# Kernel tuning notes

Hardware: AMD Instinct MI355X
Metric: run time of the kernel (lower is better)

The kernel has to match this reference:

```python
import jax, jax.numpy as jnp
import numpy as np

B, T, D_MODEL = 4, 4096, 512
HEADS, BUCKET_SIZE, N_HASHES = 8, 64, 4
DIM_HEAD = D_MODEL // HEADS  # 64
D_FFN = 2048
N_BUCKETS = T // BUCKET_SIZE  # 64
SELF_ATTN_VALUE = -5e4  # reformer TOKEN_SELF_ATTN_VALUE


def setup_inputs() -> dict:
    key = jax.random.key(0)
    ks = jax.random.split(key, 16)
    s = 0.02
    return {
        'x': jax.random.normal(ks[0], (B, T, D_MODEL), jnp.float32),
        'rotations': jax.random.normal(ks[1], (DIM_HEAD, N_HASHES, N_BUCKETS // 2), jnp.float32),
        'w_qk': jax.random.normal(ks[2], (D_MODEL, D_MODEL), jnp.float32) * s,
        'w_v': jax.random.normal(ks[3], (D_MODEL, D_MODEL), jnp.float32) * s,
        'w_out': jax.random.normal(ks[4], (D_MODEL, D_MODEL), jnp.float32) * s,
        'b_out': jnp.zeros((D_MODEL,), jnp.float32),
        'ln1_g': jnp.ones((D_MODEL,), jnp.float32),
        'ln1_b': jnp.zeros((D_MODEL,), jnp.float32),
        'w1': jax.random.normal(ks[5], (D_FFN, D_MODEL), jnp.float32) * s,
        'b1': jnp.zeros((D_FFN,), jnp.float32),
        'w2': jax.random.normal(ks[6], (D_MODEL, D_FFN), jnp.float32) * s,
        'b2': jnp.zeros((D_MODEL,), jnp.float32),
        'ln2_g': jnp.ones((D_MODEL,), jnp.float32),
        'ln2_b': jnp.zeros((D_MODEL,), jnp.float32),
    }


def layer_norm(x, g, b, eps=1e-6):
    m = x.mean(-1, keepdims=True)
    v = ((x - m) ** 2).mean(-1, keepdims=True)
    return (x - m) / jnp.sqrt(v + eps) * g + b


def look_one_back(x):
    # concat each chunk with the previous chunk (wrap-around), along in-chunk axis
    prev = jnp.roll(x, 1, axis=1)
    return jnp.concatenate([x, prev], axis=2)


def lsh_attention(qk, v, rotations):
    # qk, v: (bh, t, d) with shared-QK; rotations: (d, n_hashes, n_buckets//2)
    bh, t, d = qk.shape
    # --- hash: random rotations, argmax over [R, -R] ---
    rot = jnp.einsum('btf,fhi->bhti', qk, rotations)
    rot = jnp.concatenate([rot, -rot], axis=-1)        # (bh, H, t, n_buckets)
    buckets = jnp.argmax(rot, axis=-1)                 # (bh, H, t)
    buckets = buckets + (jnp.arange(N_HASHES) * N_BUCKETS)[None, :, None]
    buckets = buckets.reshape(bh, N_HASHES * t)
    # --- sort by (bucket, position) ---
    ticker = jnp.arange(N_HASHES * t)
    buckets_and_t = t * buckets + (ticker % t)[None, :]
    sticker = jnp.argsort(buckets_and_t, axis=-1)      # stable sort
    undo_sort = jnp.argsort(sticker, axis=-1)
    st = sticker % t                                   # original positions, sorted order
    sqk = jnp.take_along_axis(qk, st[..., None], axis=1)
    sv = jnp.take_along_axis(v, st[..., None], axis=1)
    # --- chunk: n_hashes*n_buckets chunks of bucket_size tokens ---
    n_chunks = N_HASHES * N_BUCKETS
    bq_t = st.reshape(bh, n_chunks, -1)
    bqk = sqk.reshape(bh, n_chunks, -1, d)
    bv = sv.reshape(bh, n_chunks, -1, d)
    bk = bqk / jnp.clip(jnp.linalg.norm(bqk, axis=-1, keepdims=True), 1e-6, None)
    bk = look_one_back(bk)
    bv = look_one_back(bv)
    bkv_t = look_one_back(bq_t)
    # --- local attention within chunk (+ previous chunk) ---
    dots = jnp.einsum('bcid,bcjd->bcij', bqk, bk) * (DIM_HEAD ** -0.5)
    self_mask = bq_t[..., None] == bkv_t[..., None, :]
    dots = jnp.where(self_mask, SELF_ATTN_VALUE, dots)
    logits = jax.nn.logsumexp(dots, axis=-1, keepdims=True)
    probs = jnp.exp(dots - logits)
    bo = jnp.einsum('bcij,bcjd->bcid', probs, bv)
    # --- unsort and combine hash rounds by softmax over round logits ---
    so = bo.reshape(bh, N_HASHES * t, d)
    slogits = logits.reshape(bh, N_HASHES * t)
    o = jnp.take_along_axis(so, undo_sort[..., None], axis=1).reshape(bh, N_HASHES, t, d)
    lg = jnp.take_along_axis(slogits, undo_sort, axis=1).reshape(bh, N_HASHES, t, 1)
    w = jnp.exp(lg - jax.nn.logsumexp(lg, axis=1, keepdims=True))
    return (o * w).sum(axis=1)                         # (bh, t, d)


def reference(x, rotations, w_qk, w_v, w_out, b_out, ln1_g, ln1_b, w1, b1, w2, b2, ln2_g, ln2_b):
    b, t, _ = x.shape
    qk = x @ w_qk.T
    v = x @ w_v.T

    def split_heads(u):
        return u.reshape(b, t, HEADS, DIM_HEAD).transpose(0, 2, 1, 3).reshape(b * HEADS, t, DIM_HEAD)

    attn = lsh_attention(split_heads(qk), split_heads(v), rotations)
    attn = attn.reshape(b, HEADS, t, DIM_HEAD).transpose(0, 2, 1, 3).reshape(b, t, D_MODEL)
    attn = attn @ w_out.T + b_out
    # residual + LN (dropout is identity at inference)
    h = layer_norm(attn + x, ln1_g, ln1_b)
    # position-wise FFN with its own residual + LN
    f = jax.nn.relu(h @ w1.T + b1) @ w2.T + b2
    return layer_norm(f + h, ln2_g, ln2_b)
```

## Files before the change

kernel.cpp:

```cpp
#include <hip/hip_runtime.h>
#include <stdint.h>

typedef unsigned short u16;
typedef __attribute__((ext_vector_type(4))) int   i32x4;
typedef __attribute__((ext_vector_type(4))) float f32x4;

__device__ __forceinline__ u16 f2bf(float x){
  unsigned int u = __float_as_uint(x);
  u += 0x7FFFu + ((u >> 16) & 1u);
  return (u16)(u >> 16);
}
__device__ __forceinline__ float bf2f(u16 h){
  return __uint_as_float(((unsigned int)h) << 16);
}
__device__ __forceinline__ unsigned int cvtpk_bf16(float lo, float hi){
  unsigned int r;
  asm("v_cvt_pk_bf16_f32 %0, %1, %2" : "=v"(r) : "v"(lo), "v"(hi));
  return r;
}
__device__ __forceinline__ f32x4 mfma16(i32x4 a, i32x4 b, f32x4 c){
  asm("v_mfma_f32_16x16x32_bf16 %0, %1, %2, %0" : "+v"(c) : "v"(a), "v"(b));
  return c;
}
__device__ __forceinline__ f32x4 acc_fence(f32x4 c){
  asm volatile("s_nop 7\ns_nop 7" : "+v"(c));
  return c;
}
__device__ __forceinline__ void gl_lds16(const void* g, void* l){
  unsigned long long ga = (unsigned long long)g;
  unsigned int la = (unsigned int)(unsigned long long)l;
  __builtin_amdgcn_global_load_lds((const __attribute__((address_space(1))) void*)ga,
                                   (__attribute__((address_space(3))) void*)la, 16, 0, 0);
}
__device__ __forceinline__ int xcd_swz(int f, int n){
  int chunk = n >> 3;
  return (f & 7) * chunk + (f >> 3);
}
__device__ __forceinline__ unsigned int f2mono(float v){
  unsigned int u = __float_as_uint(v);
  return u ^ ((unsigned int)((int)u >> 31) | 0x80000000u);
}
__device__ __forceinline__ float mono2f(unsigned int mu){
  unsigned int u = (mu & 0x80000000u) ? (mu ^ 0x80000000u) : ~mu;
  return __uint_as_float(u);
}
__device__ __forceinline__ unsigned long long shfl_xor_u64(unsigned long long x, int m){
  int lo = __shfl_xor((int)(unsigned int)(x & 0xFFFFFFFFull), m);
  int hi = __shfl_xor((int)(unsigned int)(x >> 32), m);
  return ((unsigned long long)(unsigned int)hi << 32) | (unsigned int)lo;
}

__global__ __launch_bounds__(256) void k_wprep(
    const float* __restrict__ x,
    const float* __restrict__ w_qk, const float* __restrict__ w_v,
    const float* __restrict__ w_out, const float* __restrict__ w1,
    const float* __restrict__ w2, const float* __restrict__ rot,
    u16* __restrict__ xh, u16* __restrict__ xl,
    u16* __restrict__ wqkh, u16* __restrict__ wqkl,
    u16* __restrict__ wvb, u16* __restrict__ wob,
    u16* __restrict__ w1b, u16* __restrict__ w2b,
    u16* __restrict__ rothi, u16* __restrict__ rotlo)
{
  const int bid = blockIdx.x;
  if (bid < 8192){
    int i = bid*256 + threadIdx.x;
    float4 v = ((const float4*)x)[i];
    ushort4 h, l;
    h.x=f2bf(v.x); l.x=f2bf(v.x - bf2f(h.x));
    h.y=f2bf(v.y); l.y=f2bf(v.y - bf2f(h.y));
    h.z=f2bf(v.z); l.z=f2bf(v.z - bf2f(h.z));
    h.w=f2bf(v.w); l.w=f2bf(v.w - bf2f(h.w));
    ((ushort4*)xh)[i]=h; ((ushort4*)xl)[i]=l;
    return;
  }
  if (bid >= 11008){
    int i = (bid - 11008)*256 + threadIdx.x;
    int d = i & 63, n = i >> 6;
    float v = rot[d*128 + n];
    u16 h = f2bf(v);
    rothi[i] = h; rotlo[i] = f2bf(v - bf2f(h));
    return;
  }
  const int i = (bid - 8192)*256 + threadIdx.x;
  if (i < 65536){
    float4 v = ((const float4*)w_qk)[i];
    ushort4 h, l;
    h.x=f2bf(v.x); l.x=f2bf(v.x - bf2f(h.x));
    h.y=f2bf(v.y); l.y=f2bf(v.y - bf2f(h.y));
    h.z=f2bf(v.z); l.z=f2bf(v.z - bf2f(h.z));
    h.w=f2bf(v.w); l.w=f2bf(v.w - bf2f(h.w));
    ((ushort4*)wqkh)[i]=h; ((ushort4*)wqkl)[i]=l;
    return;
  }
  const float* src; u16* dst; int j;
  if (i < 131072){ src = w_v;  dst = wvb; j = i - 65536; }
  else if (i < 196608){ src = w_out; dst = wob; j = i - 131072; }
  else if (i < 458752){ src = w1;   dst = w1b; j = i - 196608; }
  else { src = w2; dst = w2b; j = i - 458752; }
  float4 v = ((const float4*)src)[j];
  ushort4 o; o.x=f2bf(v.x); o.y=f2bf(v.y); o.z=f2bf(v.z); o.w=f2bf(v.w);
  ((ushort4*)dst)[j] = o;
}

__global__ __launch_bounds__(256) void k_gemm(
    const u16* __restrict__ A0, const u16* __restrict__ B0,
    const float* __restrict__ bias, u16* __restrict__ Cb,
    int M, int N, int K)
{
  const int tid = threadIdx.x;
  const int l = tid & 63, w = tid >> 6;
  const int lr = l & 15, lg = l >> 4;
  int flat = blockIdx.y * gridDim.x + blockIdx.x;
  flat = xcd_swz(flat, gridDim.x * gridDim.y);
  const int m0 = (flat / gridDim.x) * 128, n0 = (flat % gridDim.x) * 128;
  const int mbase = (w >> 1) * 64, nbase = (w & 1) * 64;

  __shared__ __align__(16) u16 As[128*64];
  __shared__ __align__(16) u16 Bs[128*64];

  f32x4 zero = {0.f,0.f,0.f,0.f};
  f32x4 acc[4][4];
  #pragma unroll
  for (int i=0;i<4;i++)
    #pragma unroll
    for (int j=0;j<4;j++) acc[i][j] = zero;

  const int row_s = tid >> 3;
  const int c16   = tid & 7;

  for (int k0 = 0; k0 < K; k0 += 64){
    #pragma unroll
    for (int q=0;q<4;q++){
      int ra = q*32 + row_s;
      int cs = c16 ^ (ra & 7);
      gl_lds16(A0 + (size_t)(m0 + ra)*K + k0 + cs*8, (char*)As + q*4096 + tid*16);
      gl_lds16(B0 + (size_t)(n0 + ra)*K + k0 + cs*8, (char*)Bs + q*4096 + tid*16);
    }
    __syncthreads();
    #pragma unroll
    for (int kk=0; kk<64; kk+=32){
      i32x4 af[4], bfr[4];
      #pragma unroll
      for (int mf=0;mf<4;mf++){
        int row = mbase + mf*16 + lr;
        af[mf] = *(const i32x4*)((const char*)As + row*128 + (((kk*2) + (lg*16)) ^ ((row&7)<<4)));
      }
      #pragma unroll
      for (int nf=0;nf<4;nf++){
        int row = nbase + nf*16 + lr;
        bfr[nf] = *(const i32x4*)((const char*)Bs + row*128 + (((kk*2) + (lg*16)) ^ ((row&7)<<4)));
      }
      #pragma unroll
      for (int mf=0;mf<4;mf++)
        #pragma unroll
        for (int nf=0;nf<4;nf++)
          acc[mf][nf] = mfma16(af[mf], bfr[nf], acc[mf][nf]);
    }
    __syncthreads();
  }

  #pragma unroll
  for (int mf=0;mf<4;mf++){
    #pragma unroll
    for (int nf=0;nf<4;nf++){
      f32x4 v = acc_fence(acc[mf][nf]);
      #pragma unroll
      for (int r=0;r<4;r++){
        int m = m0 + mbase + mf*16 + lg*4 + r;
        int n = n0 + nbase + nf*16 + lr;
        float val = fmaxf(v[r] + bias[n], 0.f);
        Cb[(size_t)m*N + n] = f2bf(val);
      }
    }
  }
}

template<int MODE>
__global__ __launch_bounds__(256, 4) void k_gemm64(
    const u16* __restrict__ A0, const u16* __restrict__ B0,
    const float* __restrict__ bias, u16* __restrict__ Cb,
    int M, int N, int K)
{
  const int tid = threadIdx.x;
  const int l = tid & 63, w = tid >> 6;
  const int lr = l & 15, lg = l >> 4;
  int flat = xcd_swz(blockIdx.x, gridDim.x);
  const int nT = N >> 7;
  const int m0 = (flat / nT) * 64, n0 = (flat % nT) * 128;

  __shared__ __align__(16) u16 As[64*64];
  __shared__ __align__(16) u16 Bs[128*64];

  f32x4 zero = {0.f,0.f,0.f,0.f};
  f32x4 acc[4][2];
  #pragma unroll
  for (int i=0;i<4;i++)
    #pragma unroll
    for (int j=0;j<2;j++) acc[i][j] = zero;

  const int row_s = tid >> 3;
  const int c8    = tid & 7;

  for (int k0 = 0; k0 < K; k0 += 64){
    #pragma unroll
    for (int q=0;q<2;q++){
      int ra = q*32 + row_s;
      int cs = c8 ^ (ra & 7);
      gl_lds16(A0 + (size_t)(m0 + ra)*K + k0 + cs*8, (char*)As + q*4096 + tid*16);
    }
    #pragma unroll
    for (int q=0;q<4;q++){
      int rb = q*32 + row_s;
      int cs = c8 ^ (rb & 7);
      gl_lds16(B0 + (size_t)(n0 + rb)*K + k0 + cs*8, (char*)Bs + q*4096 + tid*16);
    }
    __syncthreads();
    #pragma unroll
    for (int kk=0; kk<64; kk+=32){
      i32x4 af[4], bfr[2];
      #pragma unroll
      for (int mf=0;mf<4;mf++){
        int row = mf*16 + lr;
        af[mf] = *(const i32x4*)((const char*)As + row*128 + (((kk*2) + (lg*16)) ^ ((row&7)<<4)));
      }
      #pragma unroll
      for (int nf=0;nf<2;nf++){
        int row = w*32 + nf*16 + lr;
        bfr[nf] = *(const i32x4*)((const char*)Bs + row*128 + (((kk*2) + (lg*16)) ^ ((row&7)<<4)));
      }
      #pragma unroll
      for (int mf=0;mf<4;mf++)
        #pragma unroll
        for (int nf=0;nf<2;nf++)
          acc[mf][nf] = mfma16(af[mf], bfr[nf], acc[mf][nf]);
    }
    __syncthreads();
  }

  #pragma unroll
  for (int mf=0;mf<4;mf++){
    #pragma unroll
    for (int nf=0;nf<2;nf++){
      f32x4 v = acc_fence(acc[mf][nf]);
      #pragma unroll
      for (int r=0;r<4;r++){
        int m = m0 + mf*16 + lg*4 + r;
        int n = n0 + w*32 + nf*16 + lr;
        float val = v[r];
        if (MODE == 4){
          val += bias[n];
          Cb[(size_t)m*N + n] = f2bf(val);
        } else {
          int b = m >> 12, t = m & 4095, h = n >> 6, d = n & 63;
          size_t pos = (((size_t)(b*8 + h)) << 12) + t;
          Cb[pos*192 + 64 + d] = f2bf(val);
        }
      }
    }
  }
}

__global__ __launch_bounds__(256, 3) void k_gemmqk(
    const u16* __restrict__ Ah, const u16* __restrict__ Al,
    const u16* __restrict__ Bh, const u16* __restrict__ Bl,
    u16* __restrict__ kv, u16* __restrict__ qlo)
{
  const int K = 512;
  const int tid = threadIdx.x;
  const int l = tid & 63, w = tid >> 6;
  const int lr = l & 15, lg = l >> 4;
  int flat = xcd_swz(blockIdx.x, 1024);
  const int m0 = (flat >> 3) * 128, n0 = (flat & 7) * 64;
  const int mbase = w * 32;

  __shared__ __align__(16) u16 AsH[128*64];
  __shared__ __align__(16) u16 AsL[128*64];
  __shared__ __align__(16) u16 BsH[64*64];
  __shared__ __align__(16) u16 BsL[64*64];

  f32x4 zero = {0.f,0.f,0.f,0.f};
  f32x4 acc[2][4];
  #pragma unroll
  for (int i=0;i<2;i++)
    #pragma unroll
    for (int j=0;j<4;j++) acc[i][j] = zero;

  const int row_s = tid >> 3;
  const int c16   = tid & 7;

  for (int k0 = 0; k0 < K; k0 += 64){
    #pragma unroll
    for (int q=0;q<4;q++){
      int ra = q*32 + row_s;
      int cs = c16 ^ (ra & 7);
      size_t ao = (size_t)(m0 + ra)*K + k0 + cs*8;
      gl_lds16(Ah + ao, (char*)AsH + q*4096 + tid*16);
      gl_lds16(Al + ao, (char*)AsL + q*4096 + tid*16);
    }
    #pragma unroll
    for (int q=0;q<2;q++){
      int rb = q*32 + row_s;
      int cs = c16 ^ (rb & 7);
      size_t bo2 = (size_t)(n0 + rb)*K + k0 + cs*8;
      gl_lds16(Bh + bo2, (char*)BsH + q*4096 + tid*16);
      gl_lds16(Bl + bo2, (char*)BsL + q*4096 + tid*16);
    }
    __syncthreads();
    #pragma unroll
    for (int kk=0; kk<64; kk+=32){
      i32x4 ah[2], al[2], bh2[4], bl2[4];
      #pragma unroll
      for (int mf=0;mf<2;mf++){
        int row = mbase + mf*16 + lr;
        int off = (((kk*2) + (lg*16)) ^ ((row&7)<<4));
        ah[mf] = *(const i32x4*)((const char*)AsH + row*128 + off);
        al[mf] = *(const i32x4*)((const char*)AsL + row*128 + off);
      }
      #pragma unroll
      for (int nf=0;nf<4;nf++){
        int row = nf*16 + lr;
        int off = (((kk*2) + (lg*16)) ^ ((row&7)<<4));
        bh2[nf] = *(const i32x4*)((const char*)BsH + row*128 + off);
        bl2[nf] = *(const i32x4*)((const char*)BsL + row*128 + off);
      }
      #pragma unroll
      for (int mf=0;mf<2;mf++)
        #pragma unroll
        for (int nf=0;nf<4;nf++){
          acc[mf][nf] = mfma16(ah[mf], bh2[nf], acc[mf][nf]);
          acc[mf][nf] = mfma16(al[mf], bh2[nf], acc[mf][nf]);
          acc[mf][nf] = mfma16(ah[mf], bl2[nf], acc[mf][nf]);
        }
    }
    __syncthreads();
  }

  const int hh = n0 >> 6;
  #pragma unroll
  for (int mf=0;mf<2;mf++){
    f32x4 v[4];
    #pragma unroll
    for (int nf=0;nf<4;nf++) v[nf] = acc_fence(acc[mf][nf]);
    #pragma unroll
    for (int r=0;r<4;r++){
      float ss = 0.f;
      #pragma unroll
      for (int nf=0;nf<4;nf++) ss += v[nf][r]*v[nf][r];
      ss += __shfl_xor(ss, 1); ss += __shfl_xor(ss, 2);
      ss += __shfl_xor(ss, 4); ss += __shfl_xor(ss, 8);
      float scale = 0.18033688f / fmaxf(sqrtf(ss), 1e-6f);
      int m = m0 + mbase + mf*16 + lg*4 + r;
      int b = m >> 12, t = m & 4095;
      size_t pos = (((size_t)(b*8 + hh)) << 12) + t;
      #pragma unroll
      for (int nf=0;nf<4;nf++){
        float val = v[nf][r];
        u16 hbf = f2bf(val);
        int d = nf*16 + lr;
        kv [pos*192 + d]       = f2bf(val * scale);
        kv [pos*192 + 128 + d] = hbf;
        qlo[pos*64  + d]       = f2bf(val - bf2f(hbf));
      }
    }
  }
}

__global__ __launch_bounds__(256) void k_hash2(
    const u16* __restrict__ kv, const u16* __restrict__ ql,
    const u16* __restrict__ rh, const u16* __restrict__ rl,
    int* __restrict__ bkt)
{
  const int tid = threadIdx.x;
  const int l = tid & 63, w = tid >> 6, lr = l & 15, lg = l >> 4;
  __shared__ __align__(16) u16 Rh[128*64];
  __shared__ __align__(16) u16 Rl[128*64];
  {
    const int row_s = tid >> 3, c8 = tid & 7;
    #pragma unroll
    for (int q = 0; q < 4; q++){
      int ra = q*32 + row_s;
      int cs = c8 ^ (ra & 7);
      gl_lds16(rh + ra*64 + cs*8, (char*)Rh + q*4096 + tid*16);
      gl_lds16(rl + ra*64 + cs*8, (char*)Rl + q*4096 + tid*16);
    }
  }
  const int blk = xcd_swz(blockIdx.x, gridDim.x);
  const int qrow = blk*64 + w*16 + lr;
  const size_t qoff = (size_t)qrow*192 + 128;
  const size_t loff = (size_t)qrow*64;
  i32x4 qhf[2], qlf[2];
  qhf[0] = *(const i32x4*)(kv + qoff + lg*8);
  qhf[1] = *(const i32x4*)(kv + qoff + 32 + lg*8);
  qlf[0] = *(const i32x4*)(ql + loff + lg*8);
  qlf[1] = *(const i32x4*)(ql + loff + 32 + lg*8);
  __syncthreads();

  f32x4 zero = {0.f,0.f,0.f,0.f};
  f32x4 acc[8];
  #pragma unroll
  for (int i=0;i<8;i++) acc[i] = zero;
  #pragma unroll
  for (int ks = 0; ks < 2; ks++){
    #pragma unroll
    for (int nf = 0; nf < 8; nf++){
      int row = nf*16 + lr;
      int off = (ks*64 + lg*16) ^ ((row & 7) << 4);
      i32x4 rhf = *(const i32x4*)((const char*)Rh + row*128 + off);
      i32x4 rlf = *(const i32x4*)((const char*)Rl + row*128 + off);
      acc[nf] = mfma16(rhf, qhf[ks], acc[nf]);
      acc[nf] = mfma16(rlf, qhf[ks], acc[nf]);
      acc[nf] = mfma16(rhf, qlf[ks], acc[nf]);
    }
  }

  const int bh = qrow >> 12, t = qrow & 4095;
  #pragma unroll
  for (int hh = 0; hh < 4; hh++){
    f32x4 v0 = acc_fence(acc[2*hh]);
    f32x4 v1 = acc_fence(acc[2*hh+1]);
    unsigned long long kmax = 0, kmin = 0;
    #pragma unroll
    for (int r = 0; r < 4; r++){
      int j0 = lg*4 + r, j1 = 16 + lg*4 + r;
      unsigned int mu0 = f2mono(v0[r]), mu1 = f2mono(v1[r]);
      unsigned long long a = ((unsigned long long)mu0 << 32) | (unsigned int)(31 - j0);
      unsigned long long b = ((unsigned long long)mu1 << 32) | (unsigned int)(31 - j1);
      if (a > kmax) kmax = a;
      if (b > kmax) kmax = b;
      unsigned long long c = ((unsigned long long)(~mu0) << 32) | (unsigned int)(31 - j0);
      unsigned long long d = ((unsigned long long)(~mu1) << 32) | (unsigned int)(31 - j1);
      if (c > kmin) kmin = c;
      if (d > kmin) kmin = d;
    }
    #pragma unroll
    for (int msk = 16; msk < 64; msk <<= 1){
      unsigned long long o1 = shfl_xor_u64(kmax, msk); if (o1 > kmax) kmax = o1;
      unsigned long long o2 = shfl_xor_u64(kmin, msk); if (o2 > kmin) kmin = o2;
    }
    if (lg == 0){
      float vmax = mono2f((unsigned int)(kmax >> 32));
      int jmax = 31 - (int)(kmax & 0xFFFFFFFFull);
      float vmin = mono2f(~(unsigned int)(kmin >> 32));
      int jmin = 31 - (int)(kmin & 0xFFFFFFFFull);
      int bucket = (vmax >= -vmin) ? jmax : 32 + jmin;
      bkt[((size_t)(bh*4 + hh) << 12) + t] = bucket;
    }
  }
}

__global__ __launch_bounds__(64) void k_sort(const int* __restrict__ buckets, int* __restrict__ st){
  const int grp = blockIdx.x;
  const int t = threadIdx.x;
  __shared__ int bkL[4096];
  __shared__ int hist[64][65];
  __shared__ int tot[64];
  const size_t gbase = ((size_t)grp) << 12;
  for (int i=0;i<64;i++)
    bkL[i*64 + t] = buckets[gbase + i*64 + t];
  #pragma unroll
  for (int b=0;b<64;b++) hist[t][b] = 0;
  __syncthreads();
  for (int i=0;i<64;i++){
    int b = bkL[t*64 + i];
    hist[t][b]++;
  }
  __syncthreads();
  { int run = 0;
    for (int tt=0; tt<64; tt++){ int v = hist[tt][t]; hist[tt][t] = run; run += v; }
    tot[t] = run; }
  __syncthreads();
  { int v = tot[t]; int incl = v;
    #pragma unroll
    for (int d=1; d<64; d<<=1){ int n = __shfl_up(incl, d, 64); if (t >= d) incl += n; }
    tot[t] = incl - v; }
  __syncthreads();
  const size_t obase = (((size_t)(grp>>2)) << 14) + ((size_t)(grp&3) << 12);
  for (int i=0;i<64;i++){
    int e = t*64 + i;
    int b = bkL[e];
    int dest = tot[b] + hist[t][b];
    hist[t][b]++;
    st[obase + dest] = e;
  }
}

__global__ __launch_bounds__(256, 5) void k_attn(
    const u16* __restrict__ kv,
    const int* __restrict__ st, float* __restrict__ lgt_out, u16* __restrict__ bo)
{
  int flat = blockIdx.y * gridDim.x + blockIdx.x;
  flat = xcd_swz(flat, gridDim.x * gridDim.y);
  const int c = flat & 255, bh = flat >> 8;
  const int rnd = c >> 6;
  const int cprev = (c + 255) & 255;
  const int tid = threadIdx.x;
  const int l = tid & 63, w = tid >> 6, lr = l & 15, lg = l >> 4;

  __shared__ __align__(16) u16 Ks[128*64];
  __shared__ __align__(16) u16 Vt[64*128];

  const size_t stbase = ((size_t)bh) << 14;
  const size_t kvbase = (((size_t)bh) << 12) * 192;

  {
    const int rsub = l >> 3, c8 = l & 7;
    #pragma unroll
    for (int q2 = 0; q2 < 4; q2++){
      int row = w*32 + q2*8 + rsub;
      int cc = (row < 64) ? c : cprev;
      int pos = st[stbase + (cc << 6) + (row & 63)];
      int cs = c8 ^ (row & 7);
      gl_lds16(kv + kvbase + (size_t)pos*192 + cs*8,
               (char*)Ks + (w*4 + q2)*1024 + l*16);
    }
  }

  const int pos_q16 = st[stbase + (c << 6) + (w*16 + lr)];
  i32x4 qf[2];
  #pragma unroll
  for (int ks = 0; ks < 2; ks++)
    qf[ks] = *(const i32x4*)(kv + kvbase + (size_t)pos_q16*192 + 128 + ks*32 + lg*8);

  {
    const int pp = tid & 63, db = tid >> 6;
    const int q5 = pp & 15;
    const int K0 = (pp >> 4)*32 + 16*((q5 >> 1) & 1) + 4*(q5 >> 2) + 2*(q5 & 1);
    int cc0 = (K0 < 64) ? c : cprev;
    int p0 = st[stbase + (cc0 << 6) + (K0 & 63)];
    int p1 = st[stbase + (cc0 << 6) + ((K0 + 1) & 63)];
    const u16* r0 = kv + kvbase + (size_t)p0*192 + 64 + db*16;
    const u16* r1 = kv + kvbase + (size_t)p1*192 + 64 + db*16;
    uint4 a0 = *(const uint4*)r0, a1 = *(const uint4*)(r0 + 8);
    uint4 b0 = *(const uint4*)r1, b1 = *(const uint4*)(r1 + 8);
    uint av[8] = {a0.x,a0.y,a0.z,a0.w,a1.x,a1.y,a1.z,a1.w};
    uint bv[8] = {b0.x,b0.y,b0.z,b0.w,b1.x,b1.y,b1.z,b1.w};
    #pragma unroll
    for (int dd = 0; dd < 16; dd++){
      uint lo = (av[dd>>1] >> ((dd&1)*16)) & 0xFFFFu;
      uint hi = (bv[dd>>1] >> ((dd&1)*16)) & 0xFFFFu;
      int row = db*16 + dd;
      *(uint*)((char*)Vt + row*256 + ((pp*4) ^ ((row & 7) << 5))) = lo | (hi << 16);
    }
  }
  const bool bdry = (c & 63) == 0;
  int pkprev[4][4];
  if (bdry){
    #pragma unroll
    for (int nf2=0; nf2<4; nf2++)
      #pragma unroll
      for (int r=0;r<4;r++)
        pkprev[nf2][r] = st[stbase + (cprev << 6) + nf2*16 + lg*4 + r];
  }
  __syncthreads();

  f32x4 zero = {0.f,0.f,0.f,0.f};
  f32x4 s[8];
  #pragma unroll
  for (int i=0;i<8;i++) s[i] = zero;
  __builtin_amdgcn_s_setprio(1);
  #pragma unroll
  for (int ks = 0; ks < 2; ks++){
    #pragma unroll
    for (int nf = 0; nf < 8; nf++){
      int row = nf*16 + lr;
      i32x4 kf = *(const i32x4*)((const char*)Ks + row*128 + ((ks*64 + lg*16) ^ ((row&7)<<4)));
      s[nf] = mfma16(kf, qf[ks], s[nf]);
    }
  }
  __builtin_amdgcn_s_setprio(0);

  float p[8][4];
  float sum = 0.f;
  #pragma unroll
  for (int nf=0;nf<8;nf++){
    f32x4 t = acc_fence(s[nf]);
    #pragma unroll
    for (int r=0;r<4;r++){
      float e = __builtin_amdgcn_exp2f(t[r]);
      if (nf == w && (lg*4 + r) == lr) e = 0.f;
      if (nf >= 4 && bdry && pkprev[nf-4][r] == pos_q16) e = 0.f;
      p[nf][r] = e;
      sum += e;
    }
  }
  sum += __shfl_xor(sum, 16);
  sum += __shfl_xor(sum, 32);
  float lv = logf(sum);
  float inv = 1.f / sum;
  if (l < 16)
    lgt_out[((((size_t)bh) << 12) + pos_q16)*4 + rnd] = lv;

  i32x4 pa[4];
  #pragma unroll
  for (int ks=0;ks<4;ks++){
    uint w0 = cvtpk_bf16(p[2*ks][0],   p[2*ks][1]);
    uint w1 = cvtpk_bf16(p[2*ks][2],   p[2*ks][3]);
    uint w2 = cvtpk_bf16(p[2*ks+1][0], p[2*ks+1][1]);
    uint w3 = cvtpk_bf16(p[2*ks+1][2], p[2*ks+1][3]);
    i32x4 t = {(int)w0,(int)w1,(int)w2,(int)w3};
    pa[ks] = t;
  }

  f32x4 o[4];
  #pragma unroll
  for (int i=0;i<4;i++) o[i] = zero;
  __builtin_amdgcn_s_setprio(1);
  #pragma unroll
  for (int ks=0;ks<4;ks++){
    #pragma unroll
    for (int nf=0;nf<4;nf++){
      int row = nf*16 + lr;
      i32x4 vf = *(const i32x4*)((const char*)Vt + row*256 + ((ks*64 + lg*16) ^ ((row & 7) << 5)));
      o[nf] = mfma16(pa[ks], vf, o[nf]);
    }
  }
  __builtin_amdgcn_s_setprio(0);
  float invq[4]; int posq[4];
  #pragma unroll
  for (int r=0;r<4;r++){
    invq[r] = __shfl(inv, lg*4 + r, 64);
    posq[r] = __shfl(pos_q16, lg*4 + r, 64);
  }
  #pragma unroll
  for (int nf=0;nf<4;nf++){
    f32x4 ov = acc_fence(o[nf]);
    #pragma unroll
    for (int r=0;r<4;r++){
      bo[((((size_t)bh << 12) + posq[r]))*256 + rnd*64 + nf*16 + lr] = f2bf(ov[r] * invq[r]);
    }
  }
}

__global__ __launch_bounds__(256) void k_combine(const u16* __restrict__ bo, const float* __restrict__ lgt,
                                                 u16* __restrict__ attn){
  const int wid = blockIdx.x * 4 + (threadIdx.x >> 6);
  const int l = threadIdx.x & 63;
  const int bh = wid >> 12, t = wid & 4095;
  const size_t tb = (((size_t)bh) << 12) + t;
  float4 lg4 = *(const float4*)(lgt + tb*4);
  float m = fmaxf(fmaxf(lg4.x,lg4.y), fmaxf(lg4.z,lg4.w));
  float w0 = __expf(lg4.x-m), w1 = __expf(lg4.y-m), w2 = __expf(lg4.z-m), w3 = __expf(lg4.w-m);
  float inv = 1.f / (w0+w1+w2+w3);
  const u16* bp = bo + tb*256;
  float o = w0 * bf2f(bp[l]) + w1 * bf2f(bp[64+l]) + w2 * bf2f(bp[128+l]) + w3 * bf2f(bp[192+l]);
  o *= inv;
  int b = bh >> 3, h = bh & 7;
  attn[((((size_t)b) << 12) + t) * 512 + h*64 + l] = f2bf(o);
}

template<int RESF>
__global__ __launch_bounds__(256) void k_ln(const u16* __restrict__ a,
                                            const float* __restrict__ resf, const u16* __restrict__ resb,
                                            const float* __restrict__ g, const float* __restrict__ bb,
                                            float* __restrict__ of, u16* __restrict__ ob){
  const int row = blockIdx.x*4 + (threadIdx.x >> 6);
  const int l = threadIdx.x & 63;
  const size_t base = (size_t)row*512 + l*8;
  uint4 aa = *(const uint4*)(a + base);
  uint aw[4] = {aa.x, aa.y, aa.z, aa.w};
  float av[8];
  #pragma unroll
  for (int j=0;j<4;j++){
    av[2*j]   = bf2f((u16)(aw[j] & 0xFFFF));
    av[2*j+1] = bf2f((u16)(aw[j] >> 16));
  }
  float rv[8];
  if (RESF){
    float4 r0 = *(const float4*)(resf + base);
    float4 r1 = *(const float4*)(resf + base + 4);
    rv[0]=r0.x; rv[1]=r0.y; rv[2]=r0.z; rv[3]=r0.w;
    rv[4]=r1.x; rv[5]=r1.y; rv[6]=r1.z; rv[7]=r1.w;
  } else {
    uint4 rr = *(const uint4*)(resb + base);
    uint rw[4] = {rr.x, rr.y, rr.z, rr.w};
    #pragma unroll
    for (int j=0;j<4;j++){
      rv[2*j]   = bf2f((u16)(rw[j] & 0xFFFF));
      rv[2*j+1] = bf2f((u16)(rw[j] >> 16));
    }
  }
  float v[8];
  #pragma unroll
  for (int j=0;j<8;j++) v[j] = av[j] + rv[j];
  float sum = 0.f;
  #pragma unroll
  for (int j=0;j<8;j++) sum += v[j];
  #pragma unroll
  for (int msk=1; msk<64; msk<<=1) sum += __shfl_xor(sum, msk);
  float mean = sum * (1.f/512.f);
  float ss = 0.f;
  #pragma unroll
  for (int j=0;j<8;j++){ float d = v[j]-mean; ss += d*d; }
  #pragma unroll
  for (int msk=1; msk<64; msk<<=1) ss += __shfl_xor(ss, msk);
  float rstd = rsqrtf(ss * (1.f/512.f) + 1e-6f);
  float4 g0 = *(const float4*)(g + l*8),  g1 = *(const float4*)(g + l*8 + 4);
  float4 b0 = *(const float4*)(bb + l*8), b1 = *(const float4*)(bb + l*8 + 4);
  float gv[8] = {g0.x,g0.y,g0.z,g0.w,g1.x,g1.y,g1.z,g1.w};
  float bv[8] = {b0.x,b0.y,b0.z,b0.w,b1.x,b1.y,b1.z,b1.w};
  float y[8];
  #pragma unroll
  for (int j=0;j<8;j++) y[j] = (v[j]-mean)*rstd*gv[j] + bv[j];
  if (RESF){
    #pragma unroll
    for (int j=0;j<8;j++) ob[base+j] = f2bf(y[j]);
  } else {
    #pragma unroll
    for (int j=0;j<8;j++) of[base+j] = y[j];
  }
}

extern "C" void kernel_launch(void* const* d_in, const int* in_sizes, int n_in,
                              void* d_out, int out_size, void* d_ws, size_t ws_size,
                              hipStream_t stream) {
  const float* x     = (const float*)d_in[0];
  const float* rot   = (const float*)d_in[1];
  const float* w_qk  = (const float*)d_in[2];
  const float* w_v   = (const float*)d_in[3];
  const float* w_out = (const float*)d_in[4];
  const float* b_out = (const float*)d_in[5];
  const float* ln1_g = (const float*)d_in[6];
  const float* ln1_b = (const float*)d_in[7];
  const float* w1    = (const float*)d_in[8];
  const float* b1    = (const float*)d_in[9];
  const float* w2    = (const float*)d_in[10];
  const float* b2    = (const float*)d_in[11];
  const float* ln2_g = (const float*)d_in[12];
  const float* ln2_b = (const float*)d_in[13];
  float* out = (float*)d_out;

  char* p = (char*)d_ws;
  u16*   xh   = (u16*)(p);
  u16*   xl   = (u16*)(p + 16777216);
  u16*   wqkh = (u16*)(p + 33554432);
  u16*   wqkl = (u16*)(p + 34078720);
  u16*   wvb  = (u16*)(p + 34603008);
  u16*   wob  = (u16*)(p + 35127296);
  u16*   w1b  = (u16*)(p + 35651584);
  u16*   w2b  = (u16*)(p + 37748736);
  u16*   kvb  = (u16*)(p + 39845888);
  int*   bkt  = (int*)(p + 90177536);
  int*   stb  = (int*)(p + 92274688);
  float* lgt  = (float*)(p + 94371840);
  u16*   bo   = (u16*)(p + 96468992);
  u16*   qlo   = bo;
  u16*   rothi = (u16*)(p + 96468992 + 16777216);
  u16*   rotlo = (u16*)(p + 96468992 + 16777216 + 16384);
  u16*   attnc = xl;
  u16*   projb = kvb;
  u16*   fb    = xl;
  u16*   hb    = xh;
  u16*   hid   = bo;

  k_wprep<<<11040, 256, 0, stream>>>(x, w_qk, w_v, w_out, w1, w2, rot,
                                     xh, xl, wqkh, wqkl, wvb, wob, w1b, w2b, rothi, rotlo);
  k_gemmqk<<<1024, 256, 0, stream>>>(xh, xl, wqkh, wqkl, kvb, qlo);
  k_gemm64<3><<<1024, 256, 0, stream>>>(xh, wvb, nullptr, kvb, 16384, 512, 512);
  k_hash2<<<2048, 256, 0, stream>>>(kvb, qlo, rothi, rotlo, bkt);
  k_sort<<<128, 64, 0, stream>>>(bkt, stb);
  k_attn<<<dim3(256,32), 256, 0, stream>>>(kvb, stb, lgt, bo);
  k_combine<<<32768, 256, 0, stream>>>(bo, lgt, attnc);
  k_gemm64<4><<<1024, 256, 0, stream>>>(attnc, wob, b_out, projb, 16384, 512, 512);
  k_ln<1><<<4096, 256, 0, stream>>>(projb, x, nullptr, ln1_g, ln1_b, nullptr, hb);
  k_gemm<<<dim3(16,128), 256, 0, stream>>>(hb, w1b, b1, hid, 16384, 2048, 512);
  k_gemm64<4><<<1024, 256, 0, stream>>>(hid, w2b, b2, fb, 16384, 512, 2048);
  k_ln<0><<<4096, 256, 0, stream>>>(fb, nullptr, hb, ln2_g, ln2_b, out, nullptr);
}
```

Before: 286.7 us.

## Process two adjacent chunks per attention block, reusing shared K/V rows

Each attention workgroup now handles two consecutive sorted chunks instead of one. The current chunk's keys are moved into the 'previous' half of LDS, so only the new chunk's 64 rows are gathered. The next chunk's V and Q are prefetched while the current softmax runs. This halves the gather traffic for the look-one-back keys and overlaps loads with compute, at the cost of more registers (launch bounds lowered to 4 waves) and half as many blocks.

Result: no change. 288.9 us (+0.8%).

```diff
diff --git a/kernel.cpp b/kernel.cpp
--- a/kernel.cpp
+++ b/kernel.cpp
@@ -484,15 +484,12 @@
   }
 }
 
-__global__ __launch_bounds__(256, 5) void k_attn(
+__global__ __launch_bounds__(256, 4) void k_attn(
     const u16* __restrict__ kv,
     const int* __restrict__ st, float* __restrict__ lgt_out, u16* __restrict__ bo)
 {
-  int flat = blockIdx.y * gridDim.x + blockIdx.x;
-  flat = xcd_swz(flat, gridDim.x * gridDim.y);
-  const int c = flat & 255, bh = flat >> 8;
-  const int rnd = c >> 6;
-  const int cprev = (c + 255) & 255;
+  int flat = xcd_swz(blockIdx.x, 4096);
+  const int cpair = flat & 127, bh = flat >> 7;
   const int tid = threadIdx.x;
   const int l = tid & 63, w = tid >> 6, lr = l & 15, lg = l >> 4;
 
@@ -502,8 +499,15 @@
   const size_t stbase = ((size_t)bh) << 14;
   const size_t kvbase = (((size_t)bh) << 12) * 192;
 
+  const int rsub = l >> 3, c8 = l & 7;
+  const int pp = tid & 63, db = tid >> 6;
+  const int q5 = pp & 15;
+  const int K0 = (pp >> 4)*32 + 16*((q5 >> 1) & 1) + 4*(q5 >> 2) + 2*(q5 & 1);
+
+  int c = cpair*2;
+
   {
-    const int rsub = l >> 3, c8 = l & 7;
+    const int cprev = (c + 255) & 255;
     #pragma unroll
     for (int q2 = 0; q2 < 4; q2++){
       int row = w*32 + q2*8 + rsub;
@@ -513,18 +517,6 @@
       gl_lds16(kv + kvbase + (size_t)pos*192 + cs*8,
                (char*)Ks + (w*4 + q2)*1024 + l*16);
     }
-  }
-
-  const int pos_q16 = st[stbase + (c << 6) + (w*16 + lr)];
-  i32x4 qf[2];
-  #pragma unroll
-  for (int ks = 0; ks < 2; ks++)
-    qf[ks] = *(const i32x4*)(kv + kvbase + (size_t)pos_q16*192 + 128 + ks*32 + lg*8);
-
-  {
-    const int pp = tid & 63, db = tid >> 6;
-    const int q5 = pp & 15;
-    const int K0 = (pp >> 4)*32 + 16*((q5 >> 1) & 1) + 4*(q5 >> 2) + 2*(q5 & 1);
     int cc0 = (K0 < 64) ? c : cprev;
     int p0 = st[stbase + (cc0 << 6) + (K0 & 63)];
     int p1 = st[stbase + (cc0 << 6) + ((K0 + 1) & 63)];
@@ -542,9 +534,14 @@
       *(uint*)((char*)Vt + row*256 + ((pp*4) ^ ((row & 7) << 5))) = lo | (hi << 16);
     }
   }
-  const bool bdry = (c & 63) == 0;
+  int pos_q = st[stbase + (c << 6) + (w*16 + lr)];
+  i32x4 qf[2];
+  qf[0] = *(const i32x4*)(kv + kvbase + (size_t)pos_q*192 + 128 + lg*8);
+  qf[1] = *(const i32x4*)(kv + kvbase + (size_t)pos_q*192 + 128 + 32 + lg*8);
+  bool bdry = (c & 63) == 0;
   int pkprev[4][4];
   if (bdry){
+    const int cprev = (c + 255) & 255;
     #pragma unroll
     for (int nf2=0; nf2<4; nf2++)
       #pragma unroll
@@ -553,80 +550,139 @@
   }
   __syncthreads();
 
-  f32x4 zero = {0.f,0.f,0.f,0.f};
-  f32x4 s[8];
-  #pragma unroll
-  for (int i=0;i<8;i++) s[i] = zero;
-  __builtin_amdgcn_s_setprio(1);
-  #pragma unroll
-  for (int ks = 0; ks < 2; ks++){
-    #pragma unroll
-    for (int nf = 0; nf < 8; nf++){
-      int row = nf*16 + lr;
-      i32x4 kf = *(const i32x4*)((const char*)Ks + row*128 + ((ks*64 + lg*16) ^ ((row&7)<<4)));
-      s[nf] = mfma16(kf, qf[ks], s[nf]);
-    }
-  }
-  __builtin_amdgcn_s_setprio(0);
-
-  float p[8][4];
-  float sum = 0.f;
-  #pragma unroll
-  for (int nf=0;nf<8;nf++){
-    f32x4 t = acc_fence(s[nf]);
+  int pos_q_n = 0;
+  i32x4 qfn[2];
+  uint avn[8], bvn[8];
+
+  #pragma unroll
+  for (int it = 0; it < 2; ++it){
+    const int rnd = c >> 6;
+    f32x4 zero = {0.f,0.f,0.f,0.f};
+    f32x4 s[8];
+    #pragma unroll
+    for (int i=0;i<8;i++) s[i] = zero;
+    __builtin_amdgcn_s_setprio(1);
+    #pragma unroll
+    for (int ks = 0; ks < 2; ks++){
+      #pragma unroll
+      for (int nf = 0; nf < 8; nf++){
+        int row = nf*16 + lr;
+        i32x4 kf = *(const i32x4*)((const char*)Ks + row*128 + ((ks*64 + lg*16) ^ ((row&7)<<4)));
+        s[nf] = mfma16(kf, qf[ks], s[nf]);
+      }
+    }
+    __builtin_amdgcn_s_setprio(0);
+
+    if (it == 0){
+      i32x4 kmv0 = *(const i32x4*)((const char*)Ks + tid*32);
+      i32x4 kmv1 = *(const i32x4*)((const char*)Ks + tid*32 + 16);
+      __syncthreads();
+      *(i32x4*)((char*)Ks + 8192 + tid*32)      = kmv0;
+      *(i32x4*)((char*)Ks + 8192 + tid*32 + 16) = kmv1;
+      const int c1 = c + 1;
+      #pragma unroll
+      for (int q2 = 0; q2 < 4; q2++){
+        int row = w*32 + q2*8 + rsub;
+        if (row < 64){
+          int pos = st[stbase + (c1 << 6) + row];
+          int cs = c8 ^ (row & 7);
+          gl_lds16(kv + kvbase + (size_t)pos*192 + cs*8,
+                   (char*)Ks + (w*4 + q2)*1024 + l*16);
+        }
+      }
+      {
+        int cc0 = (K0 < 64) ? c1 : c;
+        int p0 = st[stbase + (cc0 << 6) + (K0 & 63)];
+        int p1 = st[stbase + (cc0 << 6) + ((K0 + 1) & 63)];
+        const u16* r0 = kv + kvbase + (size_t)p0*192 + 64 + db*16;
+        const u16* r1 = kv + kvbase + (size_t)p1*192 + 64 + db*16;
+        uint4 a0 = *(const uint4*)r0, a1 = *(const uint4*)(r0 + 8);
+        uint4 b0 = *(const uint4*)r1, b1 = *(const uint4*)(r1 + 8);
+        avn[0]=a0.x; avn[1]=a0.y; avn[2]=a0.z; avn[3]=a0.w;
+        avn[4]=a1.x; avn[5]=a1.y; avn[6]=a1.z; avn[7]=a1.w;
+        bvn[0]=b0.x; bvn[1]=b0.y; bvn[2]=b0.z; bvn[3]=b0.w;
+        bvn[4]=b1.x; bvn[5]=b1.y; bvn[6]=b1.z; bvn[7]=b1.w;
+      }
+      pos_q_n = st[stbase + (c1 << 6) + (w*16 + lr)];
+      qfn[0] = *(const i32x4*)(kv + kvbase + (size_t)pos_q_n*192 + 128 + lg*8);
+      qfn[1] = *(const i32x4*)(kv + kvbase + (size_t)pos_q_n*192 + 128 + 32 + lg*8);
+    }
+
+    float p[8][4];
+    float sum = 0.f;
+    #pragma unroll
+    for (int nf=0;nf<8;nf++){
+      f32x4 t = acc_fence(s[nf]);
+      #pragma unroll
+      for (int r=0;r<4;r++){
+        float e = __builtin_amdgcn_exp2f(t[r]);
+        if (nf == w && (lg*4 + r) == lr) e = 0.f;
+        if (nf >= 4 && bdry && pkprev[nf-4][r] == pos_q) e = 0.f;
+        p[nf][r] = e;
+        sum += e;
+      }
+    }
+    sum += __shfl_xor(sum, 16);
+    sum += __shfl_xor(sum, 32);
+    float lv = logf(sum);
+    float inv = 1.f / sum;
+    if (l < 16)
+      lgt_out[((((size_t)bh) << 12) + pos_q)*4 + rnd] = lv;
+
+    i32x4 pa[4];
+    #pragma unroll
+    for (int ks=0;ks<4;ks++){
+      uint w0 = cvtpk_bf16(p[2*ks][0],   p[2*ks][1]);
+      uint w1 = cvtpk_bf16(p[2*ks][2],   p[2*ks][3]);
+      uint w2 = cvtpk_bf16(p[2*ks+1][0], p[2*ks+1][1]);
+      uint w3 = cvtpk_bf16(p[2*ks+1][2], p[2*ks+1][3]);
+      i32x4 t = {(int)w0,(int)w1,(int)w2,(int)w3};
+      pa[ks] = t;
+    }
+
+    f32x4 o[4];
+    #pragma unroll
+    for (int i=0;i<4;i++) o[i] = zero;
+    __builtin_amdgcn_s_setprio(1);
+    #pragma unroll
+    for (int ks=0;ks<4;ks++){
+      #pragma unroll
+      for (int nf=0;nf<4;nf++){
+        int row = nf*16 + lr;
+        i32x4 vf = *(const i32x4*)((const char*)Vt + row*256 + ((ks*64 + lg*16) ^ ((row & 7) << 5)));
+        o[nf] = mfma16(pa[ks], vf, o[nf]);
+      }
+    }
+    __builtin_amdgcn_s_setprio(0);
+    float invq[4]; int posq[4];
     #pragma unroll
     for (int r=0;r<4;r++){
-      float e = __builtin_amdgcn_exp2f(t[r]);
-      if (nf == w && (lg*4 + r) == lr) e = 0.f;
-      if (nf >= 4 && bdry && pkprev[nf-4][r] == pos_q16) e = 0.f;
-      p[nf][r] = e;
-      sum += e;
-    }
-  }
-  sum += __shfl_xor(sum, 16);
-  sum += __shfl_xor(sum, 32);
-  float lv = logf(sum);
-  float inv = 1.f / sum;
-  if (l < 16)
-    lgt_out[((((size_t)bh) << 12) + pos_q16)*4 + rnd] = lv;
-
-  i32x4 pa[4];
-  #pragma unroll
-  for (int ks=0;ks<4;ks++){
-    uint w0 = cvtpk_bf16(p[2*ks][0],   p[2*ks][1]);
-    uint w1 = cvtpk_bf16(p[2*ks][2],   p[2*ks][3]);
-    uint w2 = cvtpk_bf16(p[2*ks+1][0], p[2*ks+1][1]);
-    uint w3 = cvtpk_bf16(p[2*ks+1][2], p[2*ks+1][3]);
-    i32x4 t = {(int)w0,(int)w1,(int)w2,(int)w3};
-    pa[ks] = t;
-  }
-
-  f32x4 o[4];
-  #pragma unroll
-  for (int i=0;i<4;i++) o[i] = zero;
-  __builtin_amdgcn_s_setprio(1);
-  #pragma unroll
-  for (int ks=0;ks<4;ks++){
+      invq[r] = __shfl(inv, lg*4 + r, 64);
+      posq[r] = __shfl(pos_q, lg*4 + r, 64);
+    }
     #pragma unroll
     for (int nf=0;nf<4;nf++){
-      int row = nf*16 + lr;
-      i32x4 vf = *(const i32x4*)((const char*)Vt + row*256 + ((ks*64 + lg*16) ^ ((row & 7) << 5)));
-      o[nf] = mfma16(pa[ks], vf, o[nf]);
-    }
-  }
-  __builtin_amdgcn_s_setprio(0);
-  float invq[4]; int posq[4];
-  #pragma unroll
-  for (int r=0;r<4;r++){
-    invq[r] = __shfl(inv, lg*4 + r, 64);
-    posq[r] = __shfl(pos_q16, lg*4 + r, 64);
-  }
-  #pragma unroll
-  for (int nf=0;nf<4;nf++){
-    f32x4 ov = acc_fence(o[nf]);
-    #pragma unroll
-    for (int r=0;r<4;r++){
-      bo[((((size_t)bh << 12) + posq[r]))*256 + rnd*64 + nf*16 + lr] = f2bf(ov[r] * invq[r]);
+      f32x4 ov = acc_fence(o[nf]);
+      #pragma unroll
+      for (int r=0;r<4;r++){
+        bo[((((size_t)bh << 12) + posq[r]))*256 + rnd*64 + nf*16 + lr] = f2bf(ov[r] * invq[r]);
+      }
+    }
+
+    if (it == 0){
+      __syncthreads();
+      #pragma unroll
+      for (int dd = 0; dd < 16; dd++){
+        uint lo = (avn[dd>>1] >> ((dd&1)*16)) & 0xFFFFu;
+        uint hi = (bvn[dd>>1] >> ((dd&1)*16)) & 0xFFFFu;
+        int row = db*16 + dd;
+        *(uint*)((char*)Vt + row*256 + ((pp*4) ^ ((row & 7) << 5))) = lo | (hi << 16);
+      }
+      c = c + 1;
+      pos_q = pos_q_n;
+      qf[0] = qfn[0]; qf[1] = qfn[1];
+      bdry = false;
+      __syncthreads();
     }
   }
 }
@@ -758,7 +814,7 @@
   k_gemm64<3><<<1024, 256, 0, stream>>>(xh, wvb, nullptr, kvb, 16384, 512, 512);
   k_hash2<<<2048, 256, 0, stream>>>(kvb, qlo, rothi, rotlo, bkt);
   k_sort<<<128, 64, 0, stream>>>(bkt, stb);
-  k_attn<<<dim3(256,32), 256, 0, stream>>>(kvb, stb, lgt, bo);
+  k_attn<<<4096, 256, 0, stream>>>(kvb, stb, lgt, bo);
   k_combine<<<32768, 256, 0, stream>>>(bo, lgt, attnc);
   k_gemm64<4><<<1024, 256, 0, stream>>>(attnc, wob, b_out, projb, 16384, 512, 512);
   k_ln<1><<<4096, 256, 0, stream>>>(projb, x, nullptr, ln1_g, ln1_b, nullptr, hb);
```
